# Kernel optimization log

Measured on AMD Instinct MI355X. Metric: run time of the kernel, lower is better.

Reference implementation:

```python
import jax, jax.numpy as jnp
import numpy as np

NEG_SLOPE = 0.2  # PyG GATConv default negative_slope
EPS = 1e-16      # PyG softmax denominator eps


def gat_layer(x, src, dst, W, a_src, a_dst, num_nodes):
    """One GATConv (eval mode, self-loops already appended to src/dst).
    x: [N, Fin], W: [Fin, H*C], a_src/a_dst: [H, C]. Returns [N, H, C]."""
    H, C = a_src.shape
    h = (x @ W).reshape(num_nodes, H, C)                  # [N,H,C]
    alpha_src = jnp.sum(h * a_src, axis=-1)               # [N,H]
    alpha_dst = jnp.sum(h * a_dst, axis=-1)               # [N,H]
    e = alpha_src[src] + alpha_dst[dst]                   # [E,H]
    e = jnp.where(e > 0, e, NEG_SLOPE * e)                # leaky_relu
    # segment softmax keyed by destination node
    m = jax.ops.segment_max(e, dst, num_segments=num_nodes)   # [N,H]
    ex = jnp.exp(e - m[dst])                              # [E,H]
    s = jax.ops.segment_sum(ex, dst, num_segments=num_nodes)  # [N,H]
    alpha = ex / (s[dst] + EPS)                           # [E,H]
    # weighted scatter-aggregation of source features
    msg = h[src] * alpha[..., None]                       # [E,H,C]
    out = jax.ops.segment_sum(msg, dst, num_segments=num_nodes)  # [N,H,C]
    return out


def setup_inputs() -> dict:
    key = jax.random.key(0)
    ks = jax.random.split(key, 10)
    N, E = 50000, 800000
    Fin, C1, H, Fout = 128, 32, 8, 1
    x = jax.random.normal(ks[0], (N, Fin), dtype=jnp.float32)
    edge_index = jax.random.randint(ks[1], (2, E), 0, N).astype(jnp.int64)
    sc = 0.1
    W1 = jax.random.normal(ks[2], (Fin, H * C1), dtype=jnp.float32) * sc
    att_src1 = jax.random.normal(ks[3], (H, C1), dtype=jnp.float32) * sc
    att_dst1 = jax.random.normal(ks[4], (H, C1), dtype=jnp.float32) * sc
    bias1 = jnp.zeros((H * C1,), dtype=jnp.float32)
    W2 = jax.random.normal(ks[5], (H * C1, Fout), dtype=jnp.float32) * sc
    att_src2 = jax.random.normal(ks[6], (1, Fout), dtype=jnp.float32) * sc
    att_dst2 = jax.random.normal(ks[7], (1, Fout), dtype=jnp.float32) * sc
    bias2 = jnp.zeros((Fout,), dtype=jnp.float32)
    return {"x": x, "edge_index": edge_index, "W1": W1, "att_src1": att_src1,
            "att_dst1": att_dst1, "bias1": bias1, "W2": W2, "att_src2": att_src2,
            "att_dst2": att_dst2, "bias2": bias2}


def reference(x, edge_index, W1, att_src1, att_dst1, bias1, W2, att_src2, att_dst2, bias2):
    N = x.shape[0]
    loops = jnp.arange(N, dtype=edge_index.dtype)
    src = jnp.concatenate([edge_index[0], loops])   # add_self_loops=True
    dst = jnp.concatenate([edge_index[1], loops])
    # layer 1: heads=8, concat=True
    h1 = gat_layer(x, src, dst, W1, att_src1, att_dst1, N)      # [N,H,C1]
    h1 = h1.reshape(N, -1) + bias1                               # [N,H*C1]
    h1 = jax.nn.elu(h1)
    # layer 2: heads=1, concat=False (single head -> identity mean)
    h2 = gat_layer(h1, src, dst, W2, att_src2, att_dst2, N)      # [N,1,1]
    h2 = h2.reshape(N, -1) + bias2                               # [N,1]
    return jax.nn.sigmoid(h2).squeeze(-1)                        # [N]
```

## Files before the change

kernel.cpp:

```cpp
#include <hip/hip_runtime.h>
#include <math.h>

#define NEG_SLOPE 0.2f
#define GAT_EPS 1e-16f
#define NEG_BIG -3.0e38f
#define LOG2E 1.4426950408889634f
#define MAXDEG 96
#define BCAP 6144
#define CHUNK 2048
#define PREPB 136

typedef __attribute__((ext_vector_type(8))) short short8;
typedef __attribute__((ext_vector_type(4))) float floatx4;

__device__ __forceinline__ float leaky(float v) {
    return v > 0.f ? v : NEG_SLOPE * v;
}
__device__ __forceinline__ unsigned short f2bf(float f) {
    unsigned u = __float_as_uint(f);
    unsigned r = u + 0x7FFFu + ((u >> 16) & 1u);
    return (unsigned short)(r >> 16);
}
__device__ __forceinline__ float bf2f(unsigned short h) {
    return __uint_as_float(((unsigned)h) << 16);
}

__global__ __launch_bounds__(256) void prep_scatterA(
    const float* __restrict__ W1, const float* __restrict__ a_src,
    const float* __restrict__ a_dst, unsigned short* __restrict__ w1t,
    const int* __restrict__ ei, unsigned int* __restrict__ bucket_buf,
    int* __restrict__ bucket_cnt, int E, int ET)
{
    __shared__ int lhist[256];
    __shared__ int lbase[256];
    const int t = threadIdx.x;

    if (blockIdx.x < PREPB) {
        int idx = blockIdx.x * 256 + t;
        if (idx < 128 * 256) {
            int n = idx >> 7, k = idx & 127;
            w1t[idx] = f2bf(W1[(size_t)k * 256 + n]);
        }
        if (idx < 2048) {
            int j = idx >> 7, k = idx & 127;
            const float* a = (j < 8) ? (a_src + j * 32) : (a_dst + (j - 8) * 32);
            const float* wr = W1 + (size_t)k * 256 + (j & 7) * 32;
            float s = 0.f;
            #pragma unroll
            for (int c = 0; c < 32; ++c) s += wr[c] * a[c];
            w1t[(size_t)(256 + j) * 128 + k] = f2bf(s);
        }
        return;
    }

    lhist[t] = 0;
    __syncthreads();
    const int base = (blockIdx.x - PREPB) * CHUNK;
    unsigned int pk[8]; int bk[8], rk[8]; bool v[8];
    #pragma unroll
    for (int k = 0; k < 8; ++k) {
        int i = base + k * 256 + t;
        v[k] = i < ET;
        int ii = v[k] ? i : 0;
        int src = (ii < E) ? ei[ii] : (ii - E);
        int dst = (ii < E) ? ei[E + ii] : (ii - E);
        bk[k] = dst >> 8;
        pk[k] = ((unsigned)src << 8) | (unsigned)(dst & 255);
    }
    #pragma unroll
    for (int k = 0; k < 8; ++k)
        if (v[k]) rk[k] = atomicAdd(&lhist[bk[k]], 1);
    __syncthreads();
    if (lhist[t] > 0) lbase[t] = atomicAdd(&bucket_cnt[t], lhist[t]);
    __syncthreads();
    #pragma unroll
    for (int k = 0; k < 8; ++k) {
        if (v[k]) {
            int pos = lbase[bk[k]] + rk[k];
            if (pos < BCAP) bucket_buf[(size_t)bk[k] * BCAP + pos] = pk[k];
        }
    }
}

__global__ __launch_bounds__(256) void gemm_scatterB(
    const float* __restrict__ x, const unsigned short* __restrict__ w1t,
    unsigned short* __restrict__ h1b, float* __restrict__ as1, float* __restrict__ ad1,
    const unsigned int* __restrict__ bucket_buf, const int* __restrict__ bucket_cnt,
    int* __restrict__ cnt, unsigned short* __restrict__ csr_pad,
    int N, int ntiles)
{
    __shared__ __align__(16) unsigned short Asl[64][40];
    __shared__ __align__(16) unsigned short Bsl[272][40];
    __shared__ int lcnt[256];
    const int t = threadIdx.x;

    if (blockIdx.x >= ntiles) {
        const int b = blockIdx.x - ntiles;
        lcnt[t] = 0;
        __syncthreads();
        int tot = bucket_cnt[b]; if (tot > BCAP) tot = BCAP;
        const unsigned int* bp = bucket_buf + (size_t)b * BCAP;
        for (int j = t; j < tot; j += 256) {
            unsigned int e = bp[j];
            int loc = e & 255;
            int src = (int)(e >> 8);
            int slot = atomicAdd(&lcnt[loc], 1);
            if (slot < MAXDEG)
                csr_pad[(((size_t)b << 8) | loc) * MAXDEG + slot] = (unsigned short)src;
        }
        __syncthreads();
        int node = (b << 8) | t;
        if (node < N) cnt[node] = lcnt[t];
        return;
    }

    const int row0 = blockIdx.x * 64;
    const int wave = t >> 6, lane = t & 63;
    const int l15 = lane & 15, quad = lane >> 4;

    floatx4 acc[17];
    #pragma unroll
    for (int i = 0; i < 17; ++i) acc[i] = (floatx4){0.f, 0.f, 0.f, 0.f};

    for (int kc = 0; kc < 128; kc += 32) {
        {
            int r = t >> 2, q = t & 3;
            int row = row0 + r; if (row > N - 1) row = N - 1;
            const float4* xp = (const float4*)(x + (size_t)row * 128 + kc + q * 8);
            float4 f0 = xp[0], f1 = xp[1];
            ushort4 u0, u1;
            u0.x = f2bf(f0.x); u0.y = f2bf(f0.y); u0.z = f2bf(f0.z); u0.w = f2bf(f0.w);
            u1.x = f2bf(f1.x); u1.y = f2bf(f1.y); u1.z = f2bf(f1.z); u1.w = f2bf(f1.w);
            *(ushort4*)&Asl[r][q * 8] = u0;
            *(ushort4*)&Asl[r][q * 8 + 4] = u1;
        }
        {
            #pragma unroll
            for (int q = 0; q < 4; ++q) {
                uint4 v = *(const uint4*)&w1t[(size_t)t * 128 + kc + q * 8];
                *(uint4*)&Bsl[t][q * 8] = v;
            }
            if (t < 16) {
                #pragma unroll
                for (int q = 0; q < 4; ++q) {
                    uint4 v = *(const uint4*)&w1t[(size_t)(256 + t) * 128 + kc + q * 8];
                    *(uint4*)&Bsl[256 + t][q * 8] = v;
                }
            }
        }
        __syncthreads();
        short8 a = *(const short8*)&Asl[wave * 16 + l15][quad * 8];
        #pragma unroll
        for (int nt = 0; nt < 17; ++nt) {
            short8 bb = *(const short8*)&Bsl[nt * 16 + l15][quad * 8];
            acc[nt] = __builtin_amdgcn_mfma_f32_16x16x32_bf16(a, bb, acc[nt], 0, 0, 0);
        }
        __syncthreads();
    }
    #pragma unroll
    for (int reg = 0; reg < 4; ++reg) {
        int row = row0 + wave * 16 + quad * 4 + reg;
        if (row < N) {
            unsigned short* rp = h1b + ((size_t)row << 8);
            #pragma unroll
            for (int nt = 0; nt < 16; ++nt)
                rp[nt * 16 + l15] = f2bf(acc[nt][reg]);
            float vv = acc[16][reg] * LOG2E;
            if (l15 < 8) as1[(size_t)row * 8 + l15] = vv;
            else         ad1[(size_t)row * 8 + l15 - 8] = vv;
        }
    }
}

__global__ __launch_bounds__(256) void aggr1_fused(
    const int* __restrict__ cnt, const unsigned short* __restrict__ csr_pad,
    const float* __restrict__ as1, const float* __restrict__ ad1,
    const unsigned short* __restrict__ h1b,
    const float* __restrict__ bias1, const float* __restrict__ W2,
    float* __restrict__ h2, int N)
{
    int n = blockIdx.x * 4 + (threadIdx.x >> 6);
    int lane = threadIdx.x & 63;
    if (n >= N) return;
    const size_t rs = (size_t)n * MAXDEG;
    int deg = cnt[n]; if (deg > MAXDEG) deg = MAXDEG;
    int le = lane >> 3, lh = lane & 7, hh = lane >> 3;
    float adv = ad1[(size_t)n * 8 + lh];

    int c0 = 0, c1 = 0;
    if (lane < deg)      c0 = csr_pad[rs + lane];
    if (64 + lane < deg) c1 = csr_pad[rs + 64 + lane];

    float m = NEG_BIG, s = 0.f;
    float4 acc = make_float4(0.f, 0.f, 0.f, 0.f);

    for (int j0 = 0; j0 < deg; j0 += 8) {
        int cc = (j0 < 64) ? c0 : c1;
        int bo = j0 & 63;
        int srcs[8];
        #pragma unroll
        for (int j = 0; j < 8; ++j) srcs[j] = __shfl(cc, bo + j);
        uint2 hv[8];
        #pragma unroll
        for (int j = 0; j < 8; ++j)
            hv[j] = *(const uint2*)&h1b[((size_t)srcs[j] << 8) + lane * 4];
        float av = as1[(size_t)srcs[le] * 8 + lh];
        float l = (j0 + le < deg) ? leaky(av + adv) : NEG_BIG;
        float lj[8];
        #pragma unroll
        for (int j = 0; j < 8; ++j) lj[j] = __shfl(l, (j << 3) | hh);
        float Mc = fmaxf(fmaxf(fmaxf(lj[0], lj[1]), fmaxf(lj[2], lj[3])),
                         fmaxf(fmaxf(lj[4], lj[5]), fmaxf(lj[6], lj[7])));
        if (__any(Mc > m + 8.f)) {
            float mn = fmaxf(m, Mc);
            float sc = exp2f(m - mn);
            s *= sc; acc.x *= sc; acc.y *= sc; acc.z *= sc; acc.w *= sc;
            m = mn;
        }
        #pragma unroll
        for (int j = 0; j < 8; ++j) {
            float p = exp2f(lj[j] - m);
            s += p;
            unsigned d0 = hv[j].x, d1 = hv[j].y;
            acc.x += p * __uint_as_float(d0 << 16);
            acc.y += p * __uint_as_float(d0 & 0xFFFF0000u);
            acc.z += p * __uint_as_float(d1 << 16);
            acc.w += p * __uint_as_float(d1 & 0xFFFF0000u);
        }
    }

    float inv = 1.f / (s + GAT_EPS);
    acc.x *= inv; acc.y *= inv; acc.z *= inv; acc.w *= inv;

    float4 b = *(const float4*)&bias1[lane * 4];
    acc.x += b.x; acc.y += b.y; acc.z += b.z; acc.w += b.w;
    acc.x = acc.x > 0.f ? acc.x : __expf(acc.x) - 1.f;
    acc.y = acc.y > 0.f ? acc.y : __expf(acc.y) - 1.f;
    acc.z = acc.z > 0.f ? acc.z : __expf(acc.z) - 1.f;
    acc.w = acc.w > 0.f ? acc.w : __expf(acc.w) - 1.f;
    float4 w = *(const float4*)&W2[lane * 4];
    float part = acc.x * w.x + acc.y * w.y + acc.z * w.z + acc.w * w.w;
    #pragma unroll
    for (int mask = 1; mask < 64; mask <<= 1) part += __shfl_xor(part, mask);
    if (lane == 0) h2[n] = part;
}

__global__ __launch_bounds__(256) void layer2_fused(
    const int* __restrict__ cnt, const unsigned short* __restrict__ csr_pad,
    const float* __restrict__ h2, const float* __restrict__ a_s2,
    const float* __restrict__ a_d2, const float* __restrict__ bias2,
    float* __restrict__ out, int N)
{
    int n = blockIdx.x * 16 + (threadIdx.x >> 4);
    int sl = threadIdx.x & 15;
    if (n >= N) return;
    const size_t rs = (size_t)n * MAXDEG;
    int deg = cnt[n]; if (deg > MAXDEG) deg = MAXDEG;
    float asc = a_s2[0], adc = a_d2[0];
    float hdc = h2[n] * adc;

    int k0 = sl, k1 = sl + 16;
    float hs0 = 0.f, hs1 = 0.f;
    bool v0 = k0 < deg, v1 = k1 < deg;
    if (v0) hs0 = h2[csr_pad[rs + k0]];
    if (v1) hs1 = h2[csr_pad[rs + k1]];

    float m = NEG_BIG, s = 0.f;
    if (v0) { m = leaky(hs0 * asc + hdc); s = 1.f; }
    if (v1) {
        float l = leaky(hs1 * asc + hdc);
        if (l > m) { s = s * __expf(m - l) + 1.f; m = l; }
        else       { s += __expf(l - m); }
    }
    for (int k = sl + 32; k < deg; k += 16) {
        float hs = h2[csr_pad[rs + k]];
        float l = leaky(hs * asc + hdc);
        if (l > m) { s = s * __expf(m - l) + 1.f; m = l; }
        else       { s += __expf(l - m); }
    }
    #pragma unroll
    for (int mask = 1; mask < 16; mask <<= 1) {
        float mo = __shfl_xor(m, mask);
        float so = __shfl_xor(s, mask);
        float M = fmaxf(m, mo);
        s = s * __expf(m - M) + so * __expf(mo - M);
        m = M;
    }
    float inv = 1.f / (s + GAT_EPS);

    float acc = 0.f;
    if (v0) acc += __expf(leaky(hs0 * asc + hdc) - m) * hs0;
    if (v1) acc += __expf(leaky(hs1 * asc + hdc) - m) * hs1;
    for (int k = sl + 32; k < deg; k += 16) {
        float hs = h2[csr_pad[rs + k]];
        float l = leaky(hs * asc + hdc);
        acc += __expf(l - m) * hs;
    }
    #pragma unroll
    for (int mask = 1; mask < 16; mask <<= 1) acc += __shfl_xor(acc, mask);
    if (sl == 0) {
        float z = acc * inv + bias2[0];
        out[n] = 1.f / (1.f + __expf(-z));
    }
}

extern "C" void kernel_launch(void* const* d_in, const int* in_sizes, int n_in,
                              void* d_out, int out_size, void* d_ws, size_t ws_size,
                              hipStream_t stream)
{
    const float* x      = (const float*)d_in[0];
    const int*   ei     = (const int*)  d_in[1];
    const float* W1     = (const float*)d_in[2];
    const float* a_src1 = (const float*)d_in[3];
    const float* a_dst1 = (const float*)d_in[4];
    const float* bias1  = (const float*)d_in[5];
    const float* W2     = (const float*)d_in[6];
    const float* a_s2   = (const float*)d_in[7];
    const float* a_d2   = (const float*)d_in[8];
    const float* bias2  = (const float*)d_in[9];
    float* out = (float*)d_out;

    const int N  = in_sizes[0] / 128;
    const int E  = in_sizes[1] / 2;
    const int ET = E + N;
    const int ntiles   = (N + 63) / 64;
    const int nbuckets = (N + 255) >> 8;
    const int ablocks  = (ET + CHUNK - 1) / CHUNK;

    char* wsb = (char*)d_ws;
    size_t off = 0;
    auto walloc = [&](size_t bytes) -> void* {
        void* p = wsb + off;
        off += (bytes + 255) & ~(size_t)255;
        return p;
    };
    unsigned short* w1t     = (unsigned short*)walloc((size_t)272 * 128 * 2);
    unsigned short* h1b     = (unsigned short*)walloc((size_t)N * 256 * 2);
    float*          as1     = (float*)         walloc((size_t)N * 8 * 4);
    float*          ad1     = (float*)         walloc((size_t)N * 8 * 4);
    float*          h2      = (float*)         walloc((size_t)N * 4);
    int*            cnt     = (int*)           walloc((size_t)N * 4);
    unsigned short* csr_pad = (unsigned short*)walloc((size_t)N * MAXDEG * 2);
    int*            bucket_cnt = (int*)        walloc(256 * 4);
    unsigned int*   bucket_buf = (unsigned int*)walloc((size_t)nbuckets * BCAP * 4);

    hipMemsetAsync(bucket_cnt, 0, 256 * sizeof(int), stream);

    prep_scatterA<<<PREPB + ablocks, 256, 0, stream>>>(W1, a_src1, a_dst1, w1t,
                                                       ei, bucket_buf, bucket_cnt, E, ET);

    gemm_scatterB<<<ntiles + nbuckets, 256, 0, stream>>>(x, w1t, h1b, as1, ad1,
                                                         bucket_buf, bucket_cnt,
                                                         cnt, csr_pad, N, ntiles);

    aggr1_fused<<<(N + 3) / 4, 256, 0, stream>>>(cnt, csr_pad, as1, ad1, h1b,
                                                 bias1, W2, h2, N);
    layer2_fused<<<(N + 15) / 16, 256, 0, stream>>>(cnt, csr_pad, h2,
                                                    a_s2, a_d2, bias2, out, N);
}
```

Measured before the change: 195.2 us.

## Store layer-1 features head-major and split aggregation per head with atomic reduction

The GEMM epilogue now writes h1 and the attention logits in head-major layout ([H][N][32] and [H][N]). The aggregation kernel assigns 8 lanes per node per head, with blocks indexed by head, so each head's gather touches a 16x smaller feature table. That should improve L2 locality for the random source gathers. In exchange, the per-node layer-2 projection is combined across heads with float atomicAdd into a zeroed h2, adding a memset, atomic traffic, and non-deterministic summation order. Edge indices and source logits are also loaded redundantly for each head.

After: 211.4 us. 1.08x slower.

```diff
diff --git a/kernel.cpp b/kernel.cpp
--- a/kernel.cpp
+++ b/kernel.cpp
@@ -161,13 +161,14 @@
     for (int reg = 0; reg < 4; ++reg) {
         int row = row0 + wave * 16 + quad * 4 + reg;
         if (row < N) {
-            unsigned short* rp = h1b + ((size_t)row << 8);
             #pragma unroll
-            for (int nt = 0; nt < 16; ++nt)
-                rp[nt * 16 + l15] = f2bf(acc[nt][reg]);
+            for (int nt = 0; nt < 16; ++nt) {
+                int hh = nt >> 1, cc = ((nt & 1) << 4) + l15;
+                h1b[((size_t)hh * N + row) * 32 + cc] = f2bf(acc[nt][reg]);
+            }
             float vv = acc[16][reg] * LOG2E;
-            if (l15 < 8) as1[(size_t)row * 8 + l15] = vv;
-            else         ad1[(size_t)row * 8 + l15 - 8] = vv;
+            if (l15 < 8) as1[(size_t)l15 * N + row] = vv;
+            else         ad1[(size_t)(l15 - 8) * N + row] = vv;
         }
     }
 }
@@ -179,36 +180,37 @@
     const float* __restrict__ bias1, const float* __restrict__ W2,
     float* __restrict__ h2, int N)
 {
-    int n = blockIdx.x * 4 + (threadIdx.x >> 6);
-    int lane = threadIdx.x & 63;
+    const int h = blockIdx.x & 7;
+    const int n = (blockIdx.x >> 3) * 32 + (threadIdx.x >> 3);
+    const int lane8 = threadIdx.x & 7;
     if (n >= N) return;
+    const int wbase = (threadIdx.x & 63) & ~7;
+
     const size_t rs = (size_t)n * MAXDEG;
     int deg = cnt[n]; if (deg > MAXDEG) deg = MAXDEG;
-    int le = lane >> 3, lh = lane & 7, hh = lane >> 3;
-    float adv = ad1[(size_t)n * 8 + lh];
-
-    int c0 = 0, c1 = 0;
-    if (lane < deg)      c0 = csr_pad[rs + lane];
-    if (64 + lane < deg) c1 = csr_pad[rs + 64 + lane];
+    const float* as1h = as1 + (size_t)h * N;
+    const unsigned short* h1h = h1b + ((size_t)h * N) * 32;
+    float adv = ad1[(size_t)h * N + n];
 
     float m = NEG_BIG, s = 0.f;
     float4 acc = make_float4(0.f, 0.f, 0.f, 0.f);
 
     for (int j0 = 0; j0 < deg; j0 += 8) {
-        int cc = (j0 < 64) ? c0 : c1;
-        int bo = j0 & 63;
+        bool va = (j0 + lane8) < deg;
+        int sv = 0;
+        if (va) sv = csr_pad[rs + j0 + lane8];
+        float l = NEG_BIG;
+        if (va) l = leaky(as1h[sv] + adv);
         int srcs[8];
         #pragma unroll
-        for (int j = 0; j < 8; ++j) srcs[j] = __shfl(cc, bo + j);
+        for (int j = 0; j < 8; ++j) srcs[j] = __shfl(sv, wbase + j);
         uint2 hv[8];
         #pragma unroll
         for (int j = 0; j < 8; ++j)
-            hv[j] = *(const uint2*)&h1b[((size_t)srcs[j] << 8) + lane * 4];
-        float av = as1[(size_t)srcs[le] * 8 + lh];
-        float l = (j0 + le < deg) ? leaky(av + adv) : NEG_BIG;
+            hv[j] = *(const uint2*)&h1h[((unsigned)srcs[j] << 5) + (lane8 << 2)];
         float lj[8];
         #pragma unroll
-        for (int j = 0; j < 8; ++j) lj[j] = __shfl(l, (j << 3) | hh);
+        for (int j = 0; j < 8; ++j) lj[j] = __shfl(l, wbase + j);
         float Mc = fmaxf(fmaxf(fmaxf(lj[0], lj[1]), fmaxf(lj[2], lj[3])),
                          fmaxf(fmaxf(lj[4], lj[5]), fmaxf(lj[6], lj[7])));
         if (__any(Mc > m + 8.f)) {
@@ -232,17 +234,19 @@
     float inv = 1.f / (s + GAT_EPS);
     acc.x *= inv; acc.y *= inv; acc.z *= inv; acc.w *= inv;
 
-    float4 b = *(const float4*)&bias1[lane * 4];
+    int f = h * 32 + lane8 * 4;
+    float4 b = *(const float4*)&bias1[f];
     acc.x += b.x; acc.y += b.y; acc.z += b.z; acc.w += b.w;
     acc.x = acc.x > 0.f ? acc.x : __expf(acc.x) - 1.f;
     acc.y = acc.y > 0.f ? acc.y : __expf(acc.y) - 1.f;
     acc.z = acc.z > 0.f ? acc.z : __expf(acc.z) - 1.f;
     acc.w = acc.w > 0.f ? acc.w : __expf(acc.w) - 1.f;
-    float4 w = *(const float4*)&W2[lane * 4];
+    float4 w = *(const float4*)&W2[f];
     float part = acc.x * w.x + acc.y * w.y + acc.z * w.z + acc.w * w.w;
-    #pragma unroll
-    for (int mask = 1; mask < 64; mask <<= 1) part += __shfl_xor(part, mask);
-    if (lane == 0) h2[n] = part;
+    part += __shfl_xor(part, 1);
+    part += __shfl_xor(part, 2);
+    part += __shfl_xor(part, 4);
+    if (lane8 == 0) atomicAdd(&h2[n], part);
 }
 
 __global__ __launch_bounds__(256) void layer2_fused(
@@ -326,6 +330,7 @@
     const int ntiles   = (N + 63) / 64;
     const int nbuckets = (N + 255) >> 8;
     const int ablocks  = (ET + CHUNK - 1) / CHUNK;
+    const int ngroups  = (N + 31) / 32;
 
     char* wsb = (char*)d_ws;
     size_t off = 0;
@@ -345,6 +350,7 @@
     unsigned int*   bucket_buf = (unsigned int*)walloc((size_t)nbuckets * BCAP * 4);
 
     hipMemsetAsync(bucket_cnt, 0, 256 * sizeof(int), stream);
+    hipMemsetAsync(h2, 0, (size_t)N * sizeof(float), stream);
 
     prep_scatterA<<<PREPB + ablocks, 256, 0, stream>>>(W1, a_src1, a_dst1, w1t,
                                                        ei, bucket_buf, bucket_cnt, E, ET);
@@ -353,7 +359,7 @@
                                                          bucket_buf, bucket_cnt,
                                                          cnt, csr_pad, N, ntiles);
 
-    aggr1_fused<<<(N + 3) / 4, 256, 0, stream>>>(cnt, csr_pad, as1, ad1, h1b,
+    aggr1_fused<<<ngroups * 8, 256, 0, stream>>>(cnt, csr_pad, as1, ad1, h1b,
                                                  bias1, W2, h2, N);
     layer2_fused<<<(N + 15) / 16, 256, 0, stream>>>(cnt, csr_pad, h2,
                                                     a_s2, a_d2, bias2, out, N);
```
